# Kernel optimization log

Measured on AMD Instinct MI355X. Metric: run time of the kernel, lower is better.

Reference implementation:

```python
import jax, jax.numpy as jnp
import numpy as np

D_MODEL = 1024
H = 16
D_K = D_MODEL // H
D_FF = 4096
EPS = 1e-6


def layer_norm(x, alpha, bias):
    mean = jnp.mean(x, axis=-1, keepdims=True)
    var = jnp.mean((x - mean) ** 2, axis=-1, keepdims=True)  # unbiased=False
    return alpha * (x - mean) / jnp.sqrt(var + EPS) + bias


def setup_inputs() -> dict:
    key = jax.random.key(0)
    ks = jax.random.split(key, 8)
    B, S = 4, 2048
    sd = 1.0 / np.sqrt(D_MODEL)
    x = jax.random.normal(ks[0], (B, S, D_MODEL), dtype=jnp.float32)
    src_mask = jnp.ones((B, 1, S), dtype=jnp.int32)
    wq = jax.random.normal(ks[1], (D_MODEL, D_MODEL), jnp.float32) * sd
    wk = jax.random.normal(ks[2], (D_MODEL, D_MODEL), jnp.float32) * sd
    wv = jax.random.normal(ks[3], (D_MODEL, D_MODEL), jnp.float32) * sd
    wo = jax.random.normal(ks[4], (D_MODEL, D_MODEL), jnp.float32) * sd
    w1 = jax.random.normal(ks[5], (D_FF, D_MODEL), jnp.float32) * sd
    b1 = jnp.zeros((D_FF,), jnp.float32)
    w2 = jax.random.normal(ks[6], (D_MODEL, D_FF), jnp.float32) * (1.0 / np.sqrt(D_FF))
    b2 = jnp.zeros((D_MODEL,), jnp.float32)
    ln1_a = jnp.ones((D_MODEL,), jnp.float32)
    ln1_b = jnp.zeros((D_MODEL,), jnp.float32)
    ln2_a = jnp.ones((D_MODEL,), jnp.float32)
    ln2_b = jnp.zeros((D_MODEL,), jnp.float32)
    return dict(x=x, src_mask=src_mask, wq=wq, wk=wk, wv=wv, wo=wo,
                ln1_a=ln1_a, ln1_b=ln1_b, ln2_a=ln2_a, ln2_b=ln2_b,
                w1=w1, b1=b1, w2=w2, b2=b2)


def attention(xn, wq, wk, wv, wo, src_mask):
    B, S, _ = xn.shape
    # torch nn.Linear: y = x @ W.T
    q = (xn @ wq.T).reshape(B, S, H, D_K).transpose(0, 2, 1, 3)  # [B,H,S,Dk]
    k = (xn @ wk.T).reshape(B, S, H, D_K).transpose(0, 2, 1, 3)
    v = (xn @ wv.T).reshape(B, S, H, D_K).transpose(0, 2, 1, 3)
    scores = jnp.einsum('bhqd,bhkd->bhqk', q, k) / np.sqrt(D_K)
    m = src_mask[:, None, :, :]  # [B,1,1,S] from [B,1,S]
    scores = jnp.where(m == 0, -jnp.inf, scores)
    attn = jax.nn.softmax(scores, axis=-1)
    out = jnp.einsum('bhqk,bhkd->bhqd', attn, v)
    out = out.transpose(0, 2, 1, 3).reshape(B, S, D_MODEL)
    return out @ wo.T


def reference(x, src_mask, wq, wk, wv, wo, ln1_a, ln1_b, ln2_a, ln2_b, w1, b1, w2, b2):
    # pre-LN residual 1: self-attention
    xn = layer_norm(x, ln1_a, ln1_b)
    x = x + attention(xn, wq, wk, wv, wo, src_mask)
    # pre-LN residual 2: FFN
    xn = layer_norm(x, ln2_a, ln2_b)
    h = jax.nn.relu(xn @ w1.T + b1)
    x = x + (h @ w2.T + b2)
    return x
```

## Files before the change

### kernel.cpp

```cpp
#include <hip/hip_runtime.h>
#include <stdint.h>

typedef unsigned short u16;
typedef __bf16 bf16x8 __attribute__((ext_vector_type(8)));
typedef float   f32x4 __attribute__((ext_vector_type(4)));
typedef u16     u16x8 __attribute__((ext_vector_type(8)));
typedef u16     u16x4 __attribute__((ext_vector_type(4)));

__device__ __forceinline__ float bf2f(u16 u) {
    union { uint32_t i; float f; } c; c.i = ((uint32_t)u) << 16; return c.f;
}
__device__ __forceinline__ u16 f2bf(float f) {
    union { float f; uint32_t i; } c; c.f = f;
    uint32_t r = c.i + 0x7FFFu + ((c.i >> 16) & 1u);
    return (u16)(r >> 16);
}
__device__ __forceinline__ u16 f2bf_fast(float f) {
    union { float f; uint32_t i; } c; c.f = f;
    return (u16)((c.i + 0x8000u) >> 16);
}
__device__ __forceinline__ void gload_lds16(const u16* g, u16* l) {
    __builtin_amdgcn_global_load_lds(
        (__attribute__((address_space(1))) void*)(g),
        (__attribute__((address_space(3))) void*)(l), 16, 0, 0);
}

__global__ __launch_bounds__(256) void cvt_all(
    const float* __restrict__ wq, const float* __restrict__ wk,
    const float* __restrict__ wv, const float* __restrict__ wo,
    const float* __restrict__ w1, const float* __restrict__ w2,
    u16* __restrict__ wqb, u16* __restrict__ wkb, u16* __restrict__ wvb,
    u16* __restrict__ wob, u16* __restrict__ w1b, u16* __restrict__ w2b)
{
    int blk = blockIdx.x;
    const float* src; u16* dst; int off;
    if      (blk < 1024)  { src = wq; dst = wqb; off = blk; }
    else if (blk < 2048)  { src = wk; dst = wkb; off = blk - 1024; }
    else if (blk < 3072)  { src = wv; dst = wvb; off = blk - 2048; }
    else if (blk < 4096)  { src = wo; dst = wob; off = blk - 3072; }
    else if (blk < 8192)  { src = w1; dst = w1b; off = blk - 4096; }
    else                  { src = w2; dst = w2b; off = blk - 8192; }
    int i = off * 1024 + threadIdx.x * 4;
    float4 v = *(const float4*)(src + i);
    u16x4 o; o[0] = f2bf(v.x); o[1] = f2bf(v.y); o[2] = f2bf(v.z); o[3] = f2bf(v.w);
    *(u16x4*)(dst + i) = o;
}

__global__ __launch_bounds__(256) void ln_kernel(
    const float* __restrict__ x, const float* __restrict__ ga,
    const float* __restrict__ be, u16* __restrict__ out)
{
    const int D = 1024;
    int row  = blockIdx.x * 4 + (threadIdx.x >> 6);
    int lane = threadIdx.x & 63;
    const float* xr = x + (size_t)row * D + lane * 16;
    float f[16];
#pragma unroll
    for (int i = 0; i < 4; ++i) *(float4*)&f[i * 4] = *(const float4*)(xr + i * 4);
    float s = 0.f, s2 = 0.f;
#pragma unroll
    for (int i = 0; i < 16; ++i) { s += f[i]; s2 += f[i] * f[i]; }
#pragma unroll
    for (int off = 1; off < 64; off <<= 1) {
        s  += __shfl_xor(s,  off, 64);
        s2 += __shfl_xor(s2, off, 64);
    }
    float mean = s * (1.0f / 1024.0f);
    float var  = s2 * (1.0f / 1024.0f) - mean * mean;
    var = var < 0.f ? 0.f : var;
    float inv = 1.0f / sqrtf(var + 1e-6f);
    float g[16], b[16];
#pragma unroll
    for (int i = 0; i < 4; ++i) {
        *(float4*)&g[i * 4] = *(const float4*)(ga + lane * 16 + i * 4);
        *(float4*)&b[i * 4] = *(const float4*)(be + lane * 16 + i * 4);
    }
    u16x8 o0, o1;
#pragma unroll
    for (int i = 0; i < 8; ++i) {
        o0[i] = f2bf(g[i]     * (f[i]     - mean) * inv + b[i]);
        o1[i] = f2bf(g[8 + i] * (f[8 + i] - mean) * inv + b[8 + i]);
    }
    u16* orow = out + (size_t)row * D + lane * 16;
    *(u16x8*)(orow)     = o0;
    *(u16x8*)(orow + 8) = o1;
}

__device__ __forceinline__ void gemm_core(
    const u16* __restrict__ A, const u16* __restrict__ W,
    int K, int ldw, int row_a0, int row_w0,
    u16* As, u16* Bs, f32x4 (&acc)[4][4])
{
    int tid  = threadIdx.x;
    int lane = tid & 63;
    int quad = (lane >> 4), l16 = lane & 15;
    int wave = tid >> 6;
    int wr = wave >> 1, wc = wave & 1;
    int srow = tid >> 2, scol = (tid & 3) * 8;
    const u16* a0p = A + (size_t)(row_a0 + srow) * K + scol;
    const u16* a1p = a0p + (size_t)64 * K;
    const u16* b0p = W + (size_t)(row_w0 + srow) * ldw + scol;
    const u16* b1p = b0p + (size_t)64 * ldw;
    u16* la0 = As + tid * 8;
    u16* la1 = As + 2048 + tid * 8;
    u16* la2 = As + 4096 + tid * 8;
    u16* la3 = As + 6144 + tid * 8;
    u16* lb0 = Bs + tid * 8;
    u16* lb1 = Bs + 2048 + tid * 8;
    u16* lb2 = Bs + 4096 + tid * 8;
    u16* lb3 = Bs + 6144 + tid * 8;

    for (int k0 = 0; k0 < K; k0 += 64) {
        __syncthreads();
        gload_lds16(a0p + k0,      la0);
        gload_lds16(a1p + k0,      la1);
        gload_lds16(a0p + k0 + 32, la2);
        gload_lds16(a1p + k0 + 32, la3);
        gload_lds16(b0p + k0,      lb0);
        gload_lds16(b1p + k0,      lb1);
        gload_lds16(b0p + k0 + 32, lb2);
        gload_lds16(b1p + k0 + 32, lb3);
        __syncthreads();
#pragma unroll
        for (int h = 0; h < 2; ++h) {
            const u16* Ah = As + h * 4096;
            const u16* Bh = Bs + h * 4096;
            bf16x8 af[4], bf[4];
#pragma unroll
            for (int mt = 0; mt < 4; ++mt)
                af[mt] = *(const bf16x8*)(&Ah[(wr * 64 + mt * 16 + l16) * 32 + quad * 8]);
#pragma unroll
            for (int nt = 0; nt < 4; ++nt)
                bf[nt] = *(const bf16x8*)(&Bh[(wc * 64 + nt * 16 + l16) * 32 + quad * 8]);
#pragma unroll
            for (int mt = 0; mt < 4; ++mt)
#pragma unroll
                for (int nt = 0; nt < 4; ++nt)
                    acc[mt][nt] = __builtin_amdgcn_mfma_f32_16x16x32_bf16(
                        af[mt], bf[nt], acc[mt][nt], 0, 0, 0);
        }
    }
}

template<bool OUTF32>
__global__ __launch_bounds__(256) void gemm128(
    const u16* __restrict__ A, const u16* __restrict__ W,
    const float* __restrict__ bias, const float* __restrict__ resid,
    void* __restrict__ Cp, int M, int N, int K, int ldw, int do_relu)
{
    __shared__ u16 As[128 * 64];
    __shared__ u16 Bs[128 * 64];
    int tid  = threadIdx.x;
    int lane = tid & 63, wave = tid >> 6;
    int quad = lane >> 4, l16 = lane & 15;
    int wr = wave >> 1, wc = wave & 1;
    const int row_a0 = blockIdx.x * 128, row_w0 = blockIdx.y * 128;
    f32x4 acc[4][4] = {};
    gemm_core(A, W, K, ldw, row_a0, row_w0, As, Bs, acc);
#pragma unroll
    for (int mt = 0; mt < 4; ++mt) {
#pragma unroll
        for (int nt = 0; nt < 4; ++nt) {
#pragma unroll
            for (int r = 0; r < 4; ++r) {
                int grow = row_a0 + wr * 64 + mt * 16 + quad * 4 + r;
                int gcol = row_w0 + wc * 64 + nt * 16 + l16;
                float vv = acc[mt][nt][r];
                if (bias)    vv += bias[gcol];
                if (do_relu) vv = vv > 0.f ? vv : 0.f;
                if (resid)   vv += resid[(size_t)grow * N + gcol];
                if (OUTF32) ((float*)Cp)[(size_t)grow * N + gcol] = vv;
                else        ((u16*)Cp)[(size_t)grow * N + gcol] = f2bf(vv);
            }
        }
    }
}

__global__ __launch_bounds__(256) void gemm128_qkv(
    const u16* __restrict__ A, const u16* __restrict__ Wqkv,
    u16* __restrict__ qo, u16* __restrict__ ko, u16* __restrict__ vo, int K)
{
    __shared__ u16 As[128 * 64];
    __shared__ u16 Bs[128 * 64];
    int tid  = threadIdx.x;
    int lane = tid & 63, wave = tid >> 6;
    int quad = lane >> 4, l16 = lane & 15;
    int wr = wave >> 1, wc = wave & 1;
    const int row_a0 = blockIdx.x * 128, row_w0 = blockIdx.y * 128;
    f32x4 acc[4][4] = {};
    gemm_core(A, Wqkv, K, K, row_a0, row_w0, As, Bs, acc);
    int seg = row_w0 >> 10;
    u16* dst = (seg == 0) ? qo : (seg == 1) ? ko : vo;
    int col0 = row_w0 & 1023;
#pragma unroll
    for (int mt = 0; mt < 4; ++mt) {
#pragma unroll
        for (int nt = 0; nt < 4; ++nt) {
#pragma unroll
            for (int r = 0; r < 4; ++r) {
                int grow = row_a0 + wr * 64 + mt * 16 + quad * 4 + r;
                int gcol = col0 + wc * 64 + nt * 16 + l16;
                dst[(size_t)grow * 1024 + gcol] = f2bf(acc[mt][nt][r]);
            }
        }
    }
}

__global__ __launch_bounds__(256) void attn_kernel(
    const u16* __restrict__ Q, const u16* __restrict__ Km, const u16* __restrict__ Vm,
    const int* __restrict__ mask, u16* __restrict__ O)
{
    const int S = 2048, DM = 1024;
    const float C1 = 0.18033688f;
    const float C0 = -11.541560f;
    __shared__ u16 Qs[64][72];
    __shared__ u16 Ks[64][72];
    __shared__ u16 Vt[64][72];
    __shared__ u16 Ps[64][72];

    int qt = blockIdx.x, bh = blockIdx.y;
    int b = bh >> 4, h = bh & 15;
    int tid = threadIdx.x;
    int wave = tid >> 6, lane = tid & 63;
    int quad = lane >> 4, l16 = lane & 15;
    size_t base = (size_t)b * S;
    size_t hoff = (size_t)h * 64;

    {
        int r = tid >> 2, c0 = (tid & 3) * 16;
        const u16* src = Q + (base + qt * 64 + r) * DM + hoff + c0;
        *(u16x8*)(&Qs[r][c0])     = *(const u16x8*)(src);
        *(u16x8*)(&Qs[r][c0 + 8]) = *(const u16x8*)(src + 8);
    }
    __syncthreads();
    const int q0 = wave * 16;
    bf16x8 qf0 = *(const bf16x8*)(&Qs[q0 + l16][quad * 8]);
    bf16x8 qf1 = *(const bf16x8*)(&Qs[q0 + l16][32 + quad * 8]);

    float l_r[4] = {0.f, 0.f, 0.f, 0.f};
    f32x4 o[4] = {};

    for (int k0 = 0; k0 < S; k0 += 64) {
        __syncthreads();
        {
            int key = tid >> 2, c0 = (tid & 3) * 16;
            const u16* src = Km + (base + k0 + key) * DM + hoff + c0;
            *(u16x8*)(&Ks[key][c0])     = *(const u16x8*)(src);
            *(u16x8*)(&Ks[key][c0 + 8]) = *(const u16x8*)(src + 8);
        }
        {
            int kp = tid & 31, d0 = (tid >> 5) * 8;
            const u16* s0 = Vm + (base + k0 + kp * 2) * DM + hoff + d0;
            u16x8 va = *(const u16x8*)(s0);
            u16x8 vb = *(const u16x8*)(s0 + DM);
#pragma unroll
            for (int i = 0; i < 8; ++i) {
                uint32_t w = (uint32_t)va[i] | ((uint32_t)vb[i] << 16);
                *(uint32_t*)(&Vt[d0 + i][kp * 2]) = w;
            }
        }
        __syncthreads();
        f32x4 sc[4] = {};
#pragma unroll
        for (int t = 0; t < 4; ++t) {
            int krow = 4 * l16 + t;
            bf16x8 kf0 = *(const bf16x8*)(&Ks[krow][quad * 8]);
            bf16x8 kf1 = *(const bf16x8*)(&Ks[krow][32 + quad * 8]);
            sc[t] = __builtin_amdgcn_mfma_f32_16x16x32_bf16(qf0, kf0, sc[t], 0, 0, 0);
            sc[t] = __builtin_amdgcn_mfma_f32_16x16x32_bf16(qf1, kf1, sc[t], 0, 0, 0);
        }
        int4 mk4 = *(const int4*)(mask + b * S + k0 + 4 * l16);
        float c0t[4];
        c0t[0] = (mk4.x == 0) ? -1e38f : C0;
        c0t[1] = (mk4.y == 0) ? -1e38f : C0;
        c0t[2] = (mk4.z == 0) ? -1e38f : C0;
        c0t[3] = (mk4.w == 0) ? -1e38f : C0;
#pragma unroll
        for (int r = 0; r < 4; ++r) {
            float p0 = exp2f(fmaf(sc[0][r], C1, c0t[0]));
            float p1 = exp2f(fmaf(sc[1][r], C1, c0t[1]));
            float p2 = exp2f(fmaf(sc[2][r], C1, c0t[2]));
            float p3 = exp2f(fmaf(sc[3][r], C1, c0t[3]));
            l_r[r] += (p0 + p1) + (p2 + p3);
            int prow = q0 + quad * 4 + r;
            u16x4 pw; pw[0] = f2bf_fast(p0); pw[1] = f2bf_fast(p1);
                      pw[2] = f2bf_fast(p2); pw[3] = f2bf_fast(p3);
            *(u16x4*)(&Ps[prow][4 * l16]) = pw;
        }
        bf16x8 pf0 = *(const bf16x8*)(&Ps[q0 + l16][quad * 8]);
        bf16x8 pf1 = *(const bf16x8*)(&Ps[q0 + l16][32 + quad * 8]);
#pragma unroll
        for (int t = 0; t < 4; ++t) {
            bf16x8 vf0 = *(const bf16x8*)(&Vt[t * 16 + l16][quad * 8]);
            bf16x8 vf1 = *(const bf16x8*)(&Vt[t * 16 + l16][32 + quad * 8]);
            o[t] = __builtin_amdgcn_mfma_f32_16x16x32_bf16(pf0, vf0, o[t], 0, 0, 0);
            o[t] = __builtin_amdgcn_mfma_f32_16x16x32_bf16(pf1, vf1, o[t], 0, 0, 0);
        }
    }
#pragma unroll
    for (int r = 0; r < 4; ++r) {
#pragma unroll
        for (int off = 1; off < 16; off <<= 1) l_r[r] += __shfl_xor(l_r[r], off, 16);
        float inv = 1.0f / l_r[r];
        u16* dst = O + (base + qt * 64 + q0 + quad * 4 + r) * DM + hoff + l16;
#pragma unroll
        for (int t = 0; t < 4; ++t) dst[t * 16] = f2bf(o[t][r] * inv);
    }
}

extern "C" void kernel_launch(void* const* d_in, const int* in_sizes, int n_in,
                              void* d_out, int out_size, void* d_ws, size_t ws_size,
                              hipStream_t stream)
{
    (void)in_sizes; (void)n_in; (void)out_size; (void)ws_size;
    const float* x    = (const float*)d_in[0];
    const int*   mask = (const int*)d_in[1];
    const float* wq   = (const float*)d_in[2];
    const float* wk   = (const float*)d_in[3];
    const float* wv   = (const float*)d_in[4];
    const float* wo   = (const float*)d_in[5];
    const float* ln1a = (const float*)d_in[6];
    const float* ln1b = (const float*)d_in[7];
    const float* ln2a = (const float*)d_in[8];
    const float* ln2b = (const float*)d_in[9];
    const float* w1   = (const float*)d_in[10];
    const float* b1   = (const float*)d_in[11];
    const float* w2   = (const float*)d_in[12];
    const float* b2   = (const float*)d_in[13];

    const int M = 8192, D = 1024, F = 4096;
    char* ws = (char*)d_ws;
    u16*  wqkv = (u16*)(ws);
    u16*  wqb = wqkv;
    u16*  wkb = (u16*)(ws + (2u  << 20));
    u16*  wvb = (u16*)(ws + (4u  << 20));
    u16*  wob = (u16*)(ws + (6u  << 20));
    u16*  w1b = (u16*)(ws + (8u  << 20));
    u16*  w2b = (u16*)(ws + (16u << 20));
    u16*  xn  = (u16*)(ws + (24u << 20));
    u16*  q   = (u16*)(ws + (40u << 20));
    u16*  hb  = (u16*)(ws + (40u << 20));

    u16*   kbuf = (u16*)d_out;
    u16*   vbuf = (u16*)d_out + (size_t)M * D;
    float* x1   = (float*)d_out;

    cvt_all<<<12288, 256, 0, stream>>>(wq, wk, wv, wo, w1, w2,
                                       wqb, wkb, wvb, wob, w1b, w2b);

    ln_kernel<<<M / 4, 256, 0, stream>>>(x, ln1a, ln1b, xn);
    dim3 gq(M / 128, 3072 / 128);
    gemm128_qkv<<<gq, 256, 0, stream>>>(xn, wqkv, q, kbuf, vbuf, D);
    dim3 ga(32, 64);
    attn_kernel<<<ga, 256, 0, stream>>>(q, kbuf, vbuf, mask, xn);
    dim3 g1(M / 128, D / 128);
    gemm128<true ><<<g1, 256, 0, stream>>>(xn, wob, nullptr, x, x1, M, D, D, D, 0);
    ln_kernel<<<M / 4, 256, 0, stream>>>(x1, ln2a, ln2b, xn);
    dim3 gf1(M / 128, 2048 / 128);
    dim3 gf2(M / 128, D / 128);
    gemm128<false><<<gf1, 256, 0, stream>>>(xn, w1b, b1, nullptr, hb, M, 2048, D, D, 1);
    gemm128<true ><<<gf2, 256, 0, stream>>>(hb, w2b, nullptr, x1, x1, M, D, 2048, F, 0);
    gemm128<false><<<gf1, 256, 0, stream>>>(xn, w1b + (size_t)2048 * D, b1 + 2048, nullptr, hb, M, 2048, D, D, 1);
    gemm128<true ><<<gf2, 256, 0, stream>>>(hb, w2b + 2048, b2, x1, x1, M, D, 2048, F, 0);
}
```

Measured before the change: 675.5 us.

## Double attention query tile to 128 with 8 waves and async swizzled K loads

The attention kernel now processes 128 query rows per block with 512 threads, so each K/V tile loaded into shared memory is reused by twice as many waves. K tiles are fetched directly into LDS with global_load_lds using an XOR swizzle to avoid bank conflicts, and the V transpose work is split across more threads. P is packed to bf16 with the hardware v_cvt_pk_bf16_f32 instruction. The aim is to cut global K/V traffic and per-tile load overhead, at the cost of fewer blocks and more LDS per block, which may reduce occupancy.

```diff
diff --git a/kernel.cpp b/kernel.cpp
--- a/kernel.cpp
+++ b/kernel.cpp
@@ -18,6 +18,11 @@
 __device__ __forceinline__ u16 f2bf_fast(float f) {
     union { float f; uint32_t i; } c; c.f = f;
     return (u16)((c.i + 0x8000u) >> 16);
+}
+__device__ __forceinline__ uint32_t cvt_pk_bf16(float lo, float hi) {
+    uint32_t r;
+    asm("v_cvt_pk_bf16_f32 %0, %1, %2" : "=v"(r) : "v"(lo), "v"(hi));
+    return r;
 }
 __device__ __forceinline__ void gload_lds16(const u16* g, u16* l) {
     __builtin_amdgcn_global_load_lds(
@@ -206,17 +211,17 @@
     }
 }
 
-__global__ __launch_bounds__(256) void attn_kernel(
+__global__ __launch_bounds__(512, 4) void attn_kernel(
     const u16* __restrict__ Q, const u16* __restrict__ Km, const u16* __restrict__ Vm,
     const int* __restrict__ mask, u16* __restrict__ O)
 {
     const int S = 2048, DM = 1024;
     const float C1 = 0.18033688f;
     const float C0 = -11.541560f;
-    __shared__ u16 Qs[64][72];
-    __shared__ u16 Ks[64][72];
+    __shared__ u16 Qs[128][72];
+    __shared__ u16 Ks[64 * 64];
     __shared__ u16 Vt[64][72];
-    __shared__ u16 Ps[64][72];
+    __shared__ u16 Ps[128][72];
 
     int qt = blockIdx.x, bh = blockIdx.y;
     int b = bh >> 4, h = bh & 15;
@@ -228,33 +233,37 @@
 
     {
         int r = tid >> 2, c0 = (tid & 3) * 16;
-        const u16* src = Q + (base + qt * 64 + r) * DM + hoff + c0;
+        const u16* src = Q + (base + qt * 128 + r) * DM + hoff + c0;
         *(u16x8*)(&Qs[r][c0])     = *(const u16x8*)(src);
         *(u16x8*)(&Qs[r][c0 + 8]) = *(const u16x8*)(src + 8);
     }
+    const u16* ksrc = Km + (base + (tid >> 3)) * DM + hoff
+                    + ((tid & 7) ^ ((tid >> 5) & 7)) * 8;
+    u16* kdst = Ks + tid * 8;
+    int kp = tid & 31, d0 = (tid >> 5) * 4;
+    const u16* vsrc = Vm + (base + kp * 2) * DM + hoff + d0;
+    const int* msrc = mask + b * S + 4 * l16;
+
     __syncthreads();
     const int q0 = wave * 16;
     bf16x8 qf0 = *(const bf16x8*)(&Qs[q0 + l16][quad * 8]);
     bf16x8 qf1 = *(const bf16x8*)(&Qs[q0 + l16][32 + quad * 8]);
+    const int swz = (l16 & 7) * 8;
+    const int u0  = (quad * 8) ^ swz;
 
     float l_r[4] = {0.f, 0.f, 0.f, 0.f};
     f32x4 o[4] = {};
 
-    for (int k0 = 0; k0 < S; k0 += 64) {
+    for (int it = 0; it < 32; ++it) {
         __syncthreads();
+        gload_lds16(ksrc, kdst);
+        ksrc += 64 * DM;
         {
-            int key = tid >> 2, c0 = (tid & 3) * 16;
-            const u16* src = Km + (base + k0 + key) * DM + hoff + c0;
-            *(u16x8*)(&Ks[key][c0])     = *(const u16x8*)(src);
-            *(u16x8*)(&Ks[key][c0 + 8]) = *(const u16x8*)(src + 8);
-        }
-        {
-            int kp = tid & 31, d0 = (tid >> 5) * 8;
-            const u16* s0 = Vm + (base + k0 + kp * 2) * DM + hoff + d0;
-            u16x8 va = *(const u16x8*)(s0);
-            u16x8 vb = *(const u16x8*)(s0 + DM);
-#pragma unroll
-            for (int i = 0; i < 8; ++i) {
+            u16x4 va = *(const u16x4*)(vsrc);
+            u16x4 vb = *(const u16x4*)(vsrc + DM);
+            vsrc += 64 * DM;
+#pragma unroll
+            for (int i = 0; i < 4; ++i) {
                 uint32_t w = (uint32_t)va[i] | ((uint32_t)vb[i] << 16);
                 *(uint32_t*)(&Vt[d0 + i][kp * 2]) = w;
             }
@@ -263,13 +272,13 @@
         f32x4 sc[4] = {};
 #pragma unroll
         for (int t = 0; t < 4; ++t) {
-            int krow = 4 * l16 + t;
-            bf16x8 kf0 = *(const bf16x8*)(&Ks[krow][quad * 8]);
-            bf16x8 kf1 = *(const bf16x8*)(&Ks[krow][32 + quad * 8]);
+            const u16* krp = Ks + (4 * l16 + t) * 64;
+            bf16x8 kf0 = *(const bf16x8*)(krp + u0);
+            bf16x8 kf1 = *(const bf16x8*)(krp + (u0 ^ 32));
             sc[t] = __builtin_amdgcn_mfma_f32_16x16x32_bf16(qf0, kf0, sc[t], 0, 0, 0);
             sc[t] = __builtin_amdgcn_mfma_f32_16x16x32_bf16(qf1, kf1, sc[t], 0, 0, 0);
         }
-        int4 mk4 = *(const int4*)(mask + b * S + k0 + 4 * l16);
+        int4 mk4 = *(const int4*)(msrc); msrc += 64;
         float c0t[4];
         c0t[0] = (mk4.x == 0) ? -1e38f : C0;
         c0t[1] = (mk4.y == 0) ? -1e38f : C0;
@@ -283,9 +292,10 @@
             float p3 = exp2f(fmaf(sc[3][r], C1, c0t[3]));
             l_r[r] += (p0 + p1) + (p2 + p3);
             int prow = q0 + quad * 4 + r;
-            u16x4 pw; pw[0] = f2bf_fast(p0); pw[1] = f2bf_fast(p1);
-                      pw[2] = f2bf_fast(p2); pw[3] = f2bf_fast(p3);
-            *(u16x4*)(&Ps[prow][4 * l16]) = pw;
+            uint2 pw;
+            pw.x = cvt_pk_bf16(p0, p1);
+            pw.y = cvt_pk_bf16(p2, p3);
+            *(uint2*)(&Ps[prow][4 * l16]) = pw;
         }
         bf16x8 pf0 = *(const bf16x8*)(&Ps[q0 + l16][quad * 8]);
         bf16x8 pf1 = *(const bf16x8*)(&Ps[q0 + l16][32 + quad * 8]);
@@ -302,7 +312,7 @@
 #pragma unroll
         for (int off = 1; off < 16; off <<= 1) l_r[r] += __shfl_xor(l_r[r], off, 16);
         float inv = 1.0f / l_r[r];
-        u16* dst = O + (base + qt * 64 + q0 + quad * 4 + r) * DM + hoff + l16;
+        u16* dst = O + (base + qt * 128 + q0 + quad * 4 + r) * DM + hoff + l16;
 #pragma unroll
         for (int t = 0; t < 4; ++t) dst[t * 16] = f2bf(o[t][r] * inv);
     }
@@ -351,8 +361,8 @@
     ln_kernel<<<M / 4, 256, 0, stream>>>(x, ln1a, ln1b, xn);
     dim3 gq(M / 128, 3072 / 128);
     gemm128_qkv<<<gq, 256, 0, stream>>>(xn, wqkv, q, kbuf, vbuf, D);
-    dim3 ga(32, 64);
-    attn_kernel<<<ga, 256, 0, stream>>>(q, kbuf, vbuf, mask, xn);
+    dim3 ga(2048 / 128, 64);
+    attn_kernel<<<ga, 512, 0, stream>>>(q, kbuf, vbuf, mask, xn);
     dim3 g1(M / 128, D / 128);
     gemm128<true ><<<g1, 256, 0, stream>>>(xn, wob, nullptr, x, x1, M, D, D, D, 0);
     ln_kernel<<<M / 4, 256, 0, stream>>>(x1, ln2a, ln2b, xn);
```

Result: no change. 667.2 us (-1.2%).
